# Performance work log

Hardware: AMD Instinct MI355X
Metric: run time of the kernel (lower is better)

Reference implementation:

```python
import jax, jax.numpy as jnp
import numpy as np


def _pairwise_dist(x):
    # ||xi - xj||_2 via Gram trick: sq_ij = |xi|^2 + |xj|^2 - 2 xi.xj  (exact same math,
    # avoids the O(n^2*d) broadcast intermediate of the torch code)
    sq_norms = jnp.sum(x * x, axis=1)  # [n]
    gram = x @ x.T                      # [n, n]
    sq = jnp.maximum(sq_norms[:, None] + sq_norms[None, :] - 2.0 * gram, 0.0)
    # safe sqrt: zero distance (diagonal) stays exactly 0 with well-defined grad
    pos = sq > 0
    return jnp.where(pos, jnp.sqrt(jnp.where(pos, sq, 1.0)), 0.0)


def _double_center(a):
    # A = a - colmean - rowmean + grandmean
    return a - jnp.mean(a, axis=0)[None, :] - jnp.mean(a, axis=1)[:, None] + jnp.mean(a)


def setup_inputs() -> dict:
    key = jax.random.key(0)
    kx, ky = jax.random.split(key)
    x = jax.random.normal(kx, (8192, 128), dtype=jnp.float32)
    y = jax.random.normal(ky, (8192, 128), dtype=jnp.float32)
    return {"x": x, "y": y}


def reference(x, y):
    n = x.shape[0]
    A = _double_center(_pairwise_dist(x))  # [n, n]
    B = _double_center(_pairwise_dist(y))  # [n, n]
    inv_n2 = 1.0 / float(n * n)
    dcov2_xy = jnp.sum(A * B) * inv_n2
    dcov2_xx = jnp.sum(A * A) * inv_n2
    dcov2_yy = jnp.sum(B * B) * inv_n2
    dcor = -jnp.sqrt(dcov2_xy) / jnp.sqrt(jnp.sqrt(dcov2_xx) * jnp.sqrt(dcov2_yy))
    return dcor
```

## Files before the change

kernel.cpp:

```cpp
#include <hip/hip_runtime.h>


typedef float f32x4 __attribute__((ext_vector_type(4)));
typedef __bf16 bf16x8 __attribute__((ext_vector_type(8)));
typedef __bf16 bf16x2 __attribute__((ext_vector_type(2)));

#define NR 8192
#define D 128
#define NB 128
#define NT2 8256

#define OFF_YB  2097152u
#define OFF_NX  4194304u
#define OFF_NY  (OFF_NX + 32768u)
#define OFF_RX  (OFF_NY + 32768u)
#define OFF_RY  (OFF_RX + 32768u)
#define OFF_PP  (OFF_RY + 32768u)
#define WS_NEED (OFF_PP + 198144u)

#define GLOAD_LDS16(g, l)                                                  \
    __builtin_amdgcn_global_load_lds(                                      \
        (const __attribute__((address_space(1))) unsigned*)(g),            \
        (__attribute__((address_space(3))) unsigned*)(l), 16, 0, 0)

#define WAITV(N)                                                           \
    do {                                                                   \
        asm volatile("s_waitcnt vmcnt(" #N ")" ::: "memory");              \
        __builtin_amdgcn_sched_barrier(0);                                 \
    } while (0)

__device__ __forceinline__ unsigned short bf16_rne(float f) {
    union { float f; unsigned u; } c; c.f = f;
    unsigned u = c.u;
    u += 0x7FFFu + ((u >> 16) & 1u);
    return (unsigned short)(u >> 16);
}

__global__ __launch_bounds__(256) void prep_kernel(
    const float* __restrict__ x, const float* __restrict__ y,
    unsigned short* __restrict__ xb, unsigned short* __restrict__ yb,
    float* __restrict__ nx, float* __restrict__ ny,
    float* __restrict__ Rz )
{
    int gid = blockIdx.x * 256 + threadIdx.x;
    if (gid < 2 * NR) Rz[gid] = 0.f;
    int wave = gid >> 6;
    int lane = threadIdx.x & 63;
    const float* src; unsigned short* db; float* dn; int row;
    if (wave < NR) { src = x; db = xb; dn = nx; row = wave; }
    else           { src = y; db = yb; dn = ny; row = wave - NR; }

    const float2 v = *reinterpret_cast<const float2*>(src + (size_t)row * D + lane * 2);
    float s = v.x * v.x + v.y * v.y;
    unsigned packed = (unsigned)bf16_rne(v.x) | ((unsigned)bf16_rne(v.y) << 16);
    *reinterpret_cast<unsigned*>(db + (size_t)row * D + lane * 2) = packed;
#pragma unroll
    for (int m = 1; m < 64; m <<= 1) s += __shfl_xor(s, m);
    if (lane == 0) dn[row] = s;
}

#define BSTEP(arr, S) {                                                    \
    const int b_ = (lrow >> (S)) & 1;                                      \
    _Pragma("unroll")                                                      \
    for (int i_ = 0; i_ < (8 >> (S)); ++i_) {                              \
        float k_ = b_ ? arr[2 * i_ + 1] : arr[2 * i_];                     \
        float s_ = b_ ? arr[2 * i_] : arr[2 * i_ + 1];                     \
        arr[i_] = k_ + __shfl_xor(s_, 1 << (S));                           \
    } }

__global__ __launch_bounds__(64) void dcor_wave(
    const unsigned short* __restrict__ xb, const unsigned short* __restrict__ yb,
    const float* __restrict__ nx, const float* __restrict__ ny,
    float* __restrict__ Rx, float* __restrict__ Ry,
    double* __restrict__ Pp )
{
    const int t = (blockIdx.x & 7) * (NT2 / 8) + (blockIdx.x >> 3);
    double qd = 2.0 * NB + 1.0;
    int bi = (int)((qd - sqrt(qd * qd - 8.0 * (double)t)) * 0.5);
    while (bi > 0 && bi * NB - bi * (bi - 1) / 2 > t) --bi;
    while ((bi + 1) * NB - (bi + 1) * bi / 2 <= t) ++bi;
    const int bj = bi + (t - (bi * NB - bi * (bi - 1) / 2));
    const bool diag = (bi == bj);

    __shared__ __align__(16) unsigned short Buf[2][2][64][32];
    __shared__ float nlds[4][64];

    const int lane = threadIdx.x;
    const int lrow = lane & 15, lkb = lane >> 4;

    nlds[0][lane] = nx[bi * 64 + lane];
    nlds[1][lane] = nx[bj * 64 + lane];
    nlds[2][lane] = ny[bi * 64 + lane];
    nlds[3][lane] = ny[bj * 64 + lane];
    __builtin_amdgcn_sched_barrier(0);

    auto stagec = [&](int b, const unsigned short* srcb, int kc) {
        const char* gb = (const char*)srcb;
#pragma unroll
        for (int w = 0; w < 2; ++w) {
            int blk = w ? bj : bi;
#pragma unroll
            for (int seg = 0; seg < 4; ++seg) {
                int r = seg * 16 + (lane >> 2);
                int c = (lane & 3) ^ ((r >> 1) & 3);
                const char* g = gb + (size_t)(blk * 64 + r) * 256 + kc * 64 + c * 16;
                GLOAD_LDS16(g, &Buf[b][w][seg * 16][0]);
            }
        }
    };

    const int sA = (lkb ^ ((lrow >> 1) & 3)) << 4;

    auto gram = [&](int b, f32x4 (&acc)[4][4]) {
        const char* A = (const char*)&Buf[b][0][0][0];
        const char* B = (const char*)&Buf[b][1][0][0];
        bf16x8 av[4], bv[4];
#pragma unroll
        for (int m = 0; m < 4; ++m)
            av[m] = *reinterpret_cast<const bf16x8*>(A + (m * 16 + lrow) * 64 + sA);
#pragma unroll
        for (int nf = 0; nf < 4; ++nf)
            bv[nf] = *reinterpret_cast<const bf16x8*>(B + (nf * 16 + lrow) * 64 + sA);
#pragma unroll
        for (int m = 0; m < 4; ++m)
#pragma unroll
            for (int nf = 0; nf < 4; ++nf)
                acc[m][nf] = __builtin_amdgcn_mfma_f32_16x16x32_bf16(
                    av[m], bv[nf], acc[m][nf], 0, 0, 0);
    };

    auto to_dist = [&](f32x4 (&acc)[4][4], int selR, int selC) {
        float nc[4];
#pragma unroll
        for (int nf = 0; nf < 4; ++nf) nc[nf] = nlds[selC][nf * 16 + lrow];
#pragma unroll
        for (int m = 0; m < 4; ++m) {
            const f32x4 nr4 = *reinterpret_cast<const f32x4*>(
                &nlds[selR][m * 16 + lkb * 4]);
#pragma unroll
            for (int nf = 0; nf < 4; ++nf)
#pragma unroll
                for (int r = 0; r < 4; ++r) {
                    float sq = nr4[r] + nc[nf] - 2.f * acc[m][nf][r];
                    acc[m][nf][r] = __builtin_amdgcn_sqrtf(fmaxf(sq, 0.f));
                }
        }
        if (diag) {
#pragma unroll
            for (int m = 0; m < 4; ++m)
#pragma unroll
                for (int nf = 0; nf < 4; ++nf)
#pragma unroll
                    for (int r = 0; r < 4; ++r) {
                        int row_l = m * 16 + lkb * 4 + r;
                        int col_l = nf * 16 + lrow;
                        if (row_l == col_l) acc[m][nf][r] = 0.f;
                    }
        }
    };

    const f32x4 fz = {0.f, 0.f, 0.f, 0.f};
    f32x4 accX[4][4];
#pragma unroll
    for (int m = 0; m < 4; ++m)
#pragma unroll
        for (int nf = 0; nf < 4; ++nf) accX[m][nf] = fz;

    stagec(0, xb, 0);
    stagec(1, xb, 1); WAITV(8); gram(0, accX);
    stagec(0, xb, 2); WAITV(8); gram(1, accX);
    stagec(1, xb, 3); WAITV(8); gram(0, accX);
    stagec(0, yb, 0); WAITV(8); gram(1, accX);
    to_dist(accX, 0, 1);
    unsigned dxb[32];
#pragma unroll
    for (int m = 0; m < 4; ++m)
#pragma unroll
        for (int nf = 0; nf < 4; ++nf)
#pragma unroll
            for (int rp = 0; rp < 2; ++rp) {
                bf16x2 pk;
                pk.x = (__bf16)accX[m][nf][2 * rp];
                pk.y = (__bf16)accX[m][nf][2 * rp + 1];
                dxb[(m * 4 + nf) * 2 + rp] = __builtin_bit_cast(unsigned, pk);
            }
    f32x4 accY[4][4];
#pragma unroll
    for (int m = 0; m < 4; ++m)
#pragma unroll
        for (int nf = 0; nf < 4; ++nf) accY[m][nf] = fz;
    stagec(1, yb, 1); WAITV(8); gram(0, accY);
    stagec(0, yb, 2); WAITV(8); gram(1, accY);
    stagec(1, yb, 3); WAITV(8); gram(0, accY);
    WAITV(0); gram(1, accY);
    to_dist(accY, 2, 3);

    float pxy = 0.f, pxx = 0.f, pyy = 0.f;
    float ax[16], ay[16], csx[4], csy[4];
#pragma unroll
    for (int j = 0; j < 16; ++j) { ax[j] = 0.f; ay[j] = 0.f; }
#pragma unroll
    for (int j = 0; j < 4; ++j) { csx[j] = 0.f; csy[j] = 0.f; }

#pragma unroll
    for (int m = 0; m < 4; ++m)
#pragma unroll
        for (int nf = 0; nf < 4; ++nf)
#pragma unroll
            for (int rp = 0; rp < 2; ++rp) {
                unsigned u = dxb[(m * 4 + nf) * 2 + rp];
                float dx0 = __builtin_bit_cast(float, u << 16);
                float dx1 = __builtin_bit_cast(float, u & 0xFFFF0000u);
                float dy0 = accY[m][nf][2 * rp], dy1 = accY[m][nf][2 * rp + 1];
                pxy += dx0 * dy0 + dx1 * dy1;
                pxx += dx0 * dx0 + dx1 * dx1;
                pyy += dy0 * dy0 + dy1 * dy1;
                ax[m * 4 + 2 * rp] += dx0; ax[m * 4 + 2 * rp + 1] += dx1;
                ay[m * 4 + 2 * rp] += dy0; ay[m * 4 + 2 * rp + 1] += dy1;
                csx[nf] += dx0 + dx1;      csy[nf] += dy0 + dy1;
            }

    BSTEP(ax, 0) BSTEP(ay, 0)
    BSTEP(ax, 1) BSTEP(ay, 1)
    BSTEP(ax, 2) BSTEP(ay, 2)
    BSTEP(ax, 3) BSTEP(ay, 3)
    {
        int row_l = ((lrow >> 2) << 4) + (lkb << 2) + (lrow & 3);
        atomicAdd(&Rx[bi * 64 + row_l], ax[0]);
        atomicAdd(&Ry[bi * 64 + row_l], ay[0]);
    }
#pragma unroll
    for (int nf = 0; nf < 4; ++nf) {
        float vx = csx[nf], vy = csy[nf];
        vx += __shfl_xor(vx, 16); vx += __shfl_xor(vx, 32);
        vy += __shfl_xor(vy, 16); vy += __shfl_xor(vy, 32);
        if (lkb == 0 && !diag) {
            atomicAdd(&Rx[bj * 64 + nf * 16 + lrow], vx);
            atomicAdd(&Ry[bj * 64 + nf * 16 + lrow], vy);
        }
    }
#pragma unroll
    for (int m = 1; m < 64; m <<= 1) {
        pxy += __shfl_xor(pxy, m);
        pxx += __shfl_xor(pxx, m);
        pyy += __shfl_xor(pyy, m);
    }
    if (lane == 0) {
        double sc = diag ? 1.0 : 2.0;
        Pp[t] = (double)pxy * sc;
        Pp[NT2 + t] = (double)pxx * sc;
        Pp[2 * NT2 + t] = (double)pyy * sc;
    }
}

__global__ __launch_bounds__(256) void dcor_final4(
    const float* __restrict__ Rx, const float* __restrict__ Ry,
    const double* __restrict__ Pp, unsigned* __restrict__ out)
{
    double sx = 0, sy = 0, sxy = 0, sxx = 0, syy = 0, pxy = 0, pxx = 0, pyy = 0;
    for (int i = threadIdx.x; i < NR; i += 256) {
        double rx = (double)Rx[i], ry = (double)Ry[i];
        sx += rx; sy += ry; sxy += rx * ry; sxx += rx * rx; syy += ry * ry;
    }
    for (int b = threadIdx.x; b < NT2; b += 256) {
        pxy += Pp[b]; pxx += Pp[NT2 + b]; pyy += Pp[2 * NT2 + b];
    }
    __shared__ double red[8][4];
    int lane = threadIdx.x & 63, w = threadIdx.x >> 6;
#pragma unroll
    for (int m = 1; m < 64; m <<= 1) {
        sx += __shfl_xor(sx, m);  sy += __shfl_xor(sy, m);
        sxy += __shfl_xor(sxy, m); sxx += __shfl_xor(sxx, m); syy += __shfl_xor(syy, m);
        pxy += __shfl_xor(pxy, m); pxx += __shfl_xor(pxx, m); pyy += __shfl_xor(pyy, m);
    }
    if (lane == 0) {
        red[0][w] = sx;  red[1][w] = sy;  red[2][w] = sxy; red[3][w] = sxx;
        red[4][w] = syy; red[5][w] = pxy; red[6][w] = pxx; red[7][w] = pyy;
    }
    __syncthreads();
    if (threadIdx.x == 0) {
        sx  = red[0][0] + red[0][1] + red[0][2] + red[0][3];
        sy  = red[1][0] + red[1][1] + red[1][2] + red[1][3];
        sxy = red[2][0] + red[2][1] + red[2][2] + red[2][3];
        sxx = red[3][0] + red[3][1] + red[3][2] + red[3][3];
        syy = red[4][0] + red[4][1] + red[4][2] + red[4][3];
        pxy = red[5][0] + red[5][1] + red[5][2] + red[5][3];
        pxx = red[6][0] + red[6][1] + red[6][2] + red[6][3];
        pyy = red[7][0] + red[7][1] + red[7][2] + red[7][3];
        const double inv = 1.0 / (double)NR;
        double vxy = pxy - 2.0 * inv * sxy + sx * sy * inv * inv;
        double vxx = pxx - 2.0 * inv * sxx + sx * sx * inv * inv;
        double vyy = pyy - 2.0 * inv * syy + sy * sy * inv * inv;
        vxy = fmax(vxy, 0.0);
        vxx = fmax(vxx, 1e-30); vyy = fmax(vyy, 1e-30);
        double dcor = -sqrt(vxy) / sqrt(sqrt(vxx) * sqrt(vyy));
        unsigned short b = bf16_rne((float)dcor);
        out[0] = ((unsigned)b << 16) | (unsigned)b;
    }
}

extern "C" void kernel_launch(void* const* d_in, const int* in_sizes, int n_in,
                              void* d_out, int out_size, void* d_ws, size_t ws_size,
                              hipStream_t stream)
{
    const float* x = (const float*)d_in[0];
    const float* y = (const float*)d_in[1];
    char* ws = (char*)d_ws;
    unsigned short* xb = (unsigned short*)(ws);
    unsigned short* yb = (unsigned short*)(ws + OFF_YB);
    float* nx = (float*)(ws + OFF_NX);
    float* ny = (float*)(ws + OFF_NY);
    float* Rx = (float*)(ws + OFF_RX);
    float* Ry = (float*)(ws + OFF_RY);
    double* Pp = (double*)(ws + OFF_PP);

    prep_kernel<<<4096, 256, 0, stream>>>(x, y, xb, yb, nx, ny, Rx);
    dcor_wave<<<NT2, 64, 0, stream>>>(xb, yb, nx, ny, Rx, Ry, Pp);
    dcor_final4<<<1, 256, 0, stream>>>(Rx, Ry, Pp, (unsigned*)d_out);
}
```

Baseline: 94.11 us.

## Pack two tile waves per block and use smaller k-chunks with 16x16x16 MFMA

Each 128-thread block now runs two independent waves, each processing its own upper-triangular tile, so the grid is half as large. The K dimension is staged in 16-element chunks (16 stages instead of 8 per matrix pair) with a new LDS swizzle, and the compute switches from the 16x16x32 MFMA to inline-asm 16x16x16 bf16 MFMA. Staging for the next chunk is issued immediately after each gram step, with explicit nops before the epilogue. The intent is to use a smaller LDS footprint per wave and finer-grained overlap to raise occupancy. The cost is more waits, more instructions and a lower-throughput MFMA shape.

```diff
diff --git a/kernel.cpp b/kernel.cpp
--- a/kernel.cpp
+++ b/kernel.cpp
@@ -2,13 +2,14 @@
 
 
 typedef float f32x4 __attribute__((ext_vector_type(4)));
-typedef __bf16 bf16x8 __attribute__((ext_vector_type(8)));
+typedef __bf16 bf16x4 __attribute__((ext_vector_type(4)));
 typedef __bf16 bf16x2 __attribute__((ext_vector_type(2)));
 
 #define NR 8192
 #define D 128
 #define NB 128
 #define NT2 8256
+#define NBLK 4128
 
 #define OFF_YB  2097152u
 #define OFF_NX  4194304u
@@ -28,6 +29,8 @@
         asm volatile("s_waitcnt vmcnt(" #N ")" ::: "memory");              \
         __builtin_amdgcn_sched_barrier(0);                                 \
     } while (0)
+
+#define SBARX() __builtin_amdgcn_sched_barrier(0)
 
 __device__ __forceinline__ unsigned short bf16_rne(float f) {
     union { float f; unsigned u; } c; c.f = f;
@@ -68,13 +71,15 @@
         arr[i_] = k_ + __shfl_xor(s_, 1 << (S));                           \
     } }
 
-__global__ __launch_bounds__(64) void dcor_wave(
+__global__ __launch_bounds__(128) void dcor_wave3(
     const unsigned short* __restrict__ xb, const unsigned short* __restrict__ yb,
     const float* __restrict__ nx, const float* __restrict__ ny,
     float* __restrict__ Rx, float* __restrict__ Ry,
     double* __restrict__ Pp )
 {
-    const int t = (blockIdx.x & 7) * (NT2 / 8) + (blockIdx.x >> 3);
+    const int wid = threadIdx.x >> 6, lane = threadIdx.x & 63;
+    const int bswz = (blockIdx.x & 7) * (NBLK / 8) + (blockIdx.x >> 3);
+    const int t = bswz * 2 + wid;
     double qd = 2.0 * NB + 1.0;
     int bi = (int)((qd - sqrt(qd * qd - 8.0 * (double)t)) * 0.5);
     while (bi > 0 && bi * NB - bi * (bi - 1) / 2 > t) --bi;
@@ -82,61 +87,61 @@
     const int bj = bi + (t - (bi * NB - bi * (bi - 1) / 2));
     const bool diag = (bi == bj);
 
-    __shared__ __align__(16) unsigned short Buf[2][2][64][32];
-    __shared__ float nlds[4][64];
-
-    const int lane = threadIdx.x;
+    __shared__ __align__(16) unsigned short Buf[2][2][2][64][16];
+    __shared__ float nlds[2][4][64];
+    float (*nl)[64] = nlds[wid];
+
     const int lrow = lane & 15, lkb = lane >> 4;
 
-    nlds[0][lane] = nx[bi * 64 + lane];
-    nlds[1][lane] = nx[bj * 64 + lane];
-    nlds[2][lane] = ny[bi * 64 + lane];
-    nlds[3][lane] = ny[bj * 64 + lane];
-    __builtin_amdgcn_sched_barrier(0);
-
-    auto stagec = [&](int b, const unsigned short* srcb, int kc) {
-        const char* gb = (const char*)srcb;
-#pragma unroll
-        for (int w = 0; w < 2; ++w) {
-            int blk = w ? bj : bi;
-#pragma unroll
-            for (int seg = 0; seg < 4; ++seg) {
-                int r = seg * 16 + (lane >> 2);
-                int c = (lane & 3) ^ ((r >> 1) & 3);
-                const char* g = gb + (size_t)(blk * 64 + r) * 256 + kc * 64 + c * 16;
-                GLOAD_LDS16(g, &Buf[b][w][seg * 16][0]);
+    nl[0][lane] = nx[bi * 64 + lane];
+    nl[1][lane] = nx[bj * 64 + lane];
+    nl[2][lane] = ny[bi * 64 + lane];
+    nl[3][lane] = ny[bj * 64 + lane];
+    SBARX();
+
+    auto stagec = [&](int b, int kc) {
+        const char* gb = (const char*)((kc < 8) ? xb : yb);
+        const int kk = kc & 7;
+#pragma unroll
+        for (int mat = 0; mat < 2; ++mat) {
+            int blk = mat ? bj : bi;
+#pragma unroll
+            for (int seg = 0; seg < 2; ++seg) {
+                int row = seg * 32 + (lane >> 1);
+                int g = (lane & 1) ^ ((row >> 2) & 1);
+                const char* gsrc = gb + (size_t)(blk * 64 + row) * 256 + kk * 32 + g * 16;
+                GLOAD_LDS16(gsrc, &Buf[wid][b][mat][seg * 32][0]);
             }
         }
     };
 
-    const int sA = (lkb ^ ((lrow >> 1) & 3)) << 4;
+    const int roff = lrow * 32 + (((lkb >> 1) ^ ((lrow >> 2) & 1)) << 4) + (lkb & 1) * 8;
 
     auto gram = [&](int b, f32x4 (&acc)[4][4]) {
-        const char* A = (const char*)&Buf[b][0][0][0];
-        const char* B = (const char*)&Buf[b][1][0][0];
-        bf16x8 av[4], bv[4];
+        const char* base = (const char*)&Buf[wid][b][0][0][0];
+        bf16x4 av[4], bv[4];
 #pragma unroll
         for (int m = 0; m < 4; ++m)
-            av[m] = *reinterpret_cast<const bf16x8*>(A + (m * 16 + lrow) * 64 + sA);
+            av[m] = *reinterpret_cast<const bf16x4*>(base + m * 512 + roff);
 #pragma unroll
         for (int nf = 0; nf < 4; ++nf)
-            bv[nf] = *reinterpret_cast<const bf16x8*>(B + (nf * 16 + lrow) * 64 + sA);
+            bv[nf] = *reinterpret_cast<const bf16x4*>(base + 2048 + nf * 512 + roff);
 #pragma unroll
         for (int m = 0; m < 4; ++m)
 #pragma unroll
             for (int nf = 0; nf < 4; ++nf)
-                acc[m][nf] = __builtin_amdgcn_mfma_f32_16x16x32_bf16(
-                    av[m], bv[nf], acc[m][nf], 0, 0, 0);
+                asm("v_mfma_f32_16x16x16_bf16 %0, %1, %2, %0"
+                    : "+v"(acc[m][nf]) : "v"(av[m]), "v"(bv[nf]));
     };
 
     auto to_dist = [&](f32x4 (&acc)[4][4], int selR, int selC) {
         float nc[4];
 #pragma unroll
-        for (int nf = 0; nf < 4; ++nf) nc[nf] = nlds[selC][nf * 16 + lrow];
+        for (int nf = 0; nf < 4; ++nf) nc[nf] = nl[selC][nf * 16 + lrow];
 #pragma unroll
         for (int m = 0; m < 4; ++m) {
             const f32x4 nr4 = *reinterpret_cast<const f32x4*>(
-                &nlds[selR][m * 16 + lkb * 4]);
+                &nl[selR][m * 16 + lkb * 4]);
 #pragma unroll
             for (int nf = 0; nf < 4; ++nf)
 #pragma unroll
@@ -166,11 +171,16 @@
 #pragma unroll
         for (int nf = 0; nf < 4; ++nf) accX[m][nf] = fz;
 
-    stagec(0, xb, 0);
-    stagec(1, xb, 1); WAITV(8); gram(0, accX);
-    stagec(0, xb, 2); WAITV(8); gram(1, accX);
-    stagec(1, xb, 3); WAITV(8); gram(0, accX);
-    stagec(0, yb, 0); WAITV(8); gram(1, accX);
+    stagec(0, 0); stagec(1, 1);
+    WAITV(4); gram(0, accX); SBARX(); stagec(0, 2);
+    WAITV(4); gram(1, accX); SBARX(); stagec(1, 3);
+    WAITV(4); gram(0, accX); SBARX(); stagec(0, 4);
+    WAITV(4); gram(1, accX); SBARX(); stagec(1, 5);
+    WAITV(4); gram(0, accX); SBARX(); stagec(0, 6);
+    WAITV(4); gram(1, accX); SBARX(); stagec(1, 7);
+    WAITV(4); gram(0, accX); SBARX(); stagec(0, 8);
+    WAITV(4); gram(1, accX); SBARX(); stagec(1, 9);
+    asm volatile("s_nop 7\n\ts_nop 7");
     to_dist(accX, 0, 1);
     unsigned dxb[32];
 #pragma unroll
@@ -189,10 +199,16 @@
     for (int m = 0; m < 4; ++m)
 #pragma unroll
         for (int nf = 0; nf < 4; ++nf) accY[m][nf] = fz;
-    stagec(1, yb, 1); WAITV(8); gram(0, accY);
-    stagec(0, yb, 2); WAITV(8); gram(1, accY);
-    stagec(1, yb, 3); WAITV(8); gram(0, accY);
+    SBARX();
+    WAITV(4); gram(0, accY); SBARX(); stagec(0, 10);
+    WAITV(4); gram(1, accY); SBARX(); stagec(1, 11);
+    WAITV(4); gram(0, accY); SBARX(); stagec(0, 12);
+    WAITV(4); gram(1, accY); SBARX(); stagec(1, 13);
+    WAITV(4); gram(0, accY); SBARX(); stagec(0, 14);
+    WAITV(4); gram(1, accY); SBARX(); stagec(1, 15);
+    WAITV(4); gram(0, accY);
     WAITV(0); gram(1, accY);
+    asm volatile("s_nop 7\n\ts_nop 7");
     to_dist(accY, 2, 3);
 
     float pxy = 0.f, pxx = 0.f, pyy = 0.f;
@@ -315,6 +331,6 @@
     double* Pp = (double*)(ws + OFF_PP);
 
     prep_kernel<<<4096, 256, 0, stream>>>(x, y, xb, yb, nx, ny, Rx);
-    dcor_wave<<<NT2, 64, 0, stream>>>(xb, yb, nx, ny, Rx, Ry, Pp);
+    dcor_wave3<<<NBLK, 128, 0, stream>>>(xb, yb, nx, ny, Rx, Ry, Pp);
     dcor_final4<<<1, 256, 0, stream>>>(Rx, Ry, Pp, (unsigned*)d_out);
 }
```

After: 98.23 us. +4.4%, slower.
